# Kernel tuning notes

Measured on AMD Instinct MI355X. Metric: run time of the kernel, lower is better.

## Reference

```python
import jax, jax.numpy as jnp
import numpy as np

B, S, ENC_D, DEC_D, ATTN_D, OUT_D = 32, 2048, 1024, 1024, 1024, 1024
SCALING = 1.0


def setup_inputs() -> dict:
    key = jax.random.key(0)
    ks = jax.random.split(key, 10)
    enc_states = jax.random.normal(ks[0], (B, S, ENC_D), dtype=jnp.float32)
    # lengths in [S//2, S] so every row has at least one valid position
    enc_len = jax.random.randint(ks[1], (B,), S // 2, S + 1, dtype=jnp.int32)
    dec_states = jax.random.normal(ks[2], (B, DEC_D), dtype=jnp.float32)
    s = 0.02
    W_enc = jax.random.normal(ks[3], (ENC_D, ATTN_D), dtype=jnp.float32) * s
    b_enc = jnp.zeros((ATTN_D,), dtype=jnp.float32)
    W_dec = jax.random.normal(ks[4], (DEC_D, ATTN_D), dtype=jnp.float32) * s
    b_dec = jnp.zeros((ATTN_D,), dtype=jnp.float32)
    w_attn = jax.random.normal(ks[5], (ATTN_D,), dtype=jnp.float32) * s
    W_out = jax.random.normal(ks[6], (ENC_D, OUT_D), dtype=jnp.float32) * s
    b_out = jnp.zeros((OUT_D,), dtype=jnp.float32)
    return {
        "enc_states": enc_states,
        "dec_states": dec_states,
        "W_enc": W_enc, "b_enc": b_enc,
        "W_dec": W_dec, "b_dec": b_dec,
        "w_attn": w_attn,
        "W_out": W_out, "b_out": b_out,
        "enc_len": enc_len,
    }


def reference(enc_states, dec_states, W_enc, b_enc, W_dec, b_dec, w_attn, W_out, b_out, enc_len):
    # precomputed_enc_h = mlp_enc(enc_states): [B, S, ATTN_D]
    enc_h = jnp.einsum("bse,ea->bsa", enc_states, W_enc) + b_enc
    # dec_h = mlp_dec(dec_states): [B, ATTN_D]
    dec_h = dec_states @ W_dec + b_dec
    # additive (Bahdanau) score: tanh(enc_h + dec_h) . w_attn -> [B, S]
    attn = jnp.einsum("bsa,a->bs", jnp.tanh(enc_h + dec_h[:, None, :]), w_attn)
    # length mask
    mask = jnp.arange(enc_states.shape[1])[None, :] < enc_len[:, None]  # [B, S]
    attn = jnp.where(mask, attn, -jnp.inf)
    attn = jax.nn.softmax(attn * SCALING, axis=-1)
    # context = attn @ enc_states -> [B, ENC_D]
    context = jnp.einsum("bs,bse->be", attn, enc_states)
    context = context @ W_out + b_out
    return (context, attn)
```

## Files before the change

kernel.cpp:

```cpp
#include <hip/hip_runtime.h>
#include <cstdint>
#include <cstddef>

#define BATCH 32
#define SEQ   2048
#define DIM   1024
#define MROWS (BATCH*SEQ)

typedef __attribute__((ext_vector_type(4))) float  floatx4;
typedef __attribute__((ext_vector_type(8))) short  short8;

__device__ __forceinline__ unsigned short f2bf(float f) {
  unsigned int u = __float_as_uint(f);
  u += 0x7fffu + ((u >> 16) & 1u);
  return (unsigned short)(u >> 16);
}

__device__ __forceinline__ void async16(const void* g, void* l) {
  __builtin_amdgcn_global_load_lds(
      (const __attribute__((address_space(1))) unsigned int*)g,
      (__attribute__((address_space(3))) unsigned int*)l, 16, 0, 0);
}

__device__ __forceinline__ float fast_tanh(float x) {
  float e = __expf(2.0f * x);
  return 1.0f - 2.0f * __builtin_amdgcn_rcpf(1.0f + e);
}

__global__ void k_convert(const float* __restrict__ enc, const int* __restrict__ enc_len,
                          unsigned short* __restrict__ Abf) {
  int b = blockIdx.y;
  int r0 = blockIdx.x * 8;
  if (r0 >= enc_len[b]) return;
  size_t base = ((size_t)b * SEQ + r0) * DIM;
  const float4* src = (const float4*)(enc + base);
  ushort4* dst = (ushort4*)(Abf + base);
  int tid = threadIdx.x;
#pragma unroll
  for (int i = 0; i < 8; ++i) {
    float4 v = src[tid + i * 256];
    ushort4 h;
    h.x = f2bf(v.x); h.y = f2bf(v.y); h.z = f2bf(v.z); h.w = f2bf(v.w);
    dst[tid + i * 256] = h;
  }
}

__global__ void k_transpose(const float* __restrict__ W, unsigned short* __restrict__ Wt) {
  __shared__ float tile[32][33];
  int n0 = blockIdx.x * 32, k0 = blockIdx.y * 32;
  int tx = threadIdx.x, ty = threadIdx.y;
#pragma unroll
  for (int i = 0; i < 4; ++i) {
    int y = ty + i * 8;
    tile[y][tx] = W[(size_t)(k0 + y) * DIM + n0 + tx];
  }
  __syncthreads();
#pragma unroll
  for (int i = 0; i < 4; ++i) {
    int y = ty + i * 8;
    Wt[(size_t)(n0 + y) * DIM + k0 + tx] = f2bf(tile[tx][y]);
  }
}

__global__ void k_dech(const float* __restrict__ dec, const float* __restrict__ W_dec,
                       const float* __restrict__ b_dec, const float* __restrict__ b_enc,
                       float* __restrict__ dech) {
  int a  = blockIdx.x * 256 + threadIdx.x;
  int bg = blockIdx.y * 8;
  int z  = blockIdx.z;
  float bias = (z == 0) ? (b_dec[a] + b_enc[a]) : 0.0f;
  float acc[8];
#pragma unroll
  for (int j = 0; j < 8; ++j) acc[j] = bias;
  const float* wc = W_dec + (size_t)z * 128 * DIM + a;
#pragma unroll 4
  for (int e = 0; e < 128; ++e) {
    float w = wc[(size_t)e * DIM];
#pragma unroll
    for (int j = 0; j < 8; ++j)
      acc[j] = fmaf(dec[(size_t)(bg + j) * DIM + z * 128 + e], w, acc[j]);
  }
#pragma unroll
  for (int j = 0; j < 8; ++j)
    atomicAdd(&dech[(size_t)(bg + j) * DIM + a], acc[j]);
}

#define PH_BAR do { asm volatile("" ::: "memory"); __builtin_amdgcn_s_barrier(); asm volatile("" ::: "memory"); } while(0)
#define SCHED0 __builtin_amdgcn_sched_barrier(0)
#define SP1 __builtin_amdgcn_s_setprio(1)
#define SP0 __builtin_amdgcn_s_setprio(0)
#define VMCNT(n) asm volatile("s_waitcnt vmcnt(" #n ")" ::: "memory")

__global__ void __launch_bounds__(512, 2) k_gemm256(
    const unsigned short* __restrict__ Abf,
    const unsigned short* __restrict__ Wt,
    const float* __restrict__ dech,
    const float* __restrict__ w_attn,
    const int* __restrict__ enc_len,
    float* __restrict__ score)
{
  int bid = blockIdx.x;
  int t  = (bid & 7) * 128 + (bid >> 3);
  int nb = t & 3;
  int rt = t >> 2;
  int bb = rt >> 3;
  int len = enc_len[bb];
  if (((rt & 7) * 256) >= len) return;

  __shared__ __align__(16) char lds[131072];

  int tid = threadIdx.x;
  int w = tid >> 6, lane = tid & 63;
  int wr = w >> 2;
  int wc = w & 3;
  int li = lane & 15, g = lane >> 4;
  int xl = (li & 7) << 4;

  const char* Ag = (const char*)(Abf + (size_t)rt * 256 * DIM);
  const char* Bg = (const char*)(Wt  + (size_t)nb * 256 * DIM);

  size_t sbase = (size_t)((lane >> 3) * 2048 +
                 (((lane & 7) << 4) ^ (((lane >> 3) & 7) << 4)));
  size_t swoff = (size_t)(w * 2) * 16384;
  int    ldbase = w * 2048;

#define STAGE_A(buf, h, kt) do { \
  async16(Ag + sbase + swoff + (size_t)(h) * 262144 + (size_t)(kt) * 128, \
          lds + (buf) * 32768 + ldbase + (h) * 16384); \
  async16(Ag + sbase + swoff + 16384 + (size_t)(h) * 262144 + (size_t)(kt) * 128, \
          lds + (buf) * 32768 + ldbase + 1024 + (h) * 16384); \
} while (0)
#define STAGE_B(buf, h, kt) do { \
  async16(Bg + sbase + swoff + (size_t)(h) * 262144 + (size_t)(kt) * 128, \
          lds + 65536 + (buf) * 32768 + ldbase + (h) * 16384); \
  async16(Bg + sbase + swoff + 16384 + (size_t)(h) * 262144 + (size_t)(kt) * 128, \
          lds + 65536 + (buf) * 32768 + ldbase + 1024 + (h) * 16384); \
} while (0)

  short8 sA0[2][2], sA1[2][2];
  short8 aX[2][2];
  short8 bX[2][2];
  floatx4 acc[8][4] = {};

#define RD_A2(buf, f0, DST) do { \
  const char* base_ = lds + (buf) * 32768 + (wr * 128 + (f0) * 16 + li) * 128; \
  int c0_ = (g * 16) ^ xl; \
  _Pragma("unroll") for (int j = 0; j < 2; ++j) { \
    DST[j][0] = *(const short8*)(base_ + j * 2048 + c0_); \
    DST[j][1] = *(const short8*)(base_ + j * 2048 + (c0_ ^ 64)); \
  } \
} while (0)
#define RD_B(buf, nh, DST) do { \
  const char* base_ = lds + 65536 + (buf) * 32768 + (wc * 64 + (nh) * 32 + li) * 128; \
  int c0_ = (g * 16) ^ xl; \
  _Pragma("unroll") for (int tnq = 0; tnq < 2; ++tnq) { \
    DST[tnq][0] = *(const short8*)(base_ + tnq * 2048 + c0_); \
    DST[tnq][1] = *(const short8*)(base_ + tnq * 2048 + (c0_ ^ 64)); \
  } \
} while (0)
#define MFMA_Q(mh, nh, ALO, AHI, BB) do { \
  _Pragma("unroll") for (int ks = 0; ks < 2; ++ks) \
  _Pragma("unroll") for (int tnq = 0; tnq < 2; ++tnq) { \
    acc[(mh)*4+0][(nh)*2+tnq] = __builtin_amdgcn_mfma_f32_16x16x32_bf16(ALO[0][ks], BB[tnq][ks], acc[(mh)*4+0][(nh)*2+tnq], 0, 0, 0); \
    acc[(mh)*4+1][(nh)*2+tnq] = __builtin_amdgcn_mfma_f32_16x16x32_bf16(ALO[1][ks], BB[tnq][ks], acc[(mh)*4+1][(nh)*2+tnq], 0, 0, 0); \
    acc[(mh)*4+2][(nh)*2+tnq] = __builtin_amdgcn_mfma_f32_16x16x32_bf16(AHI[0][ks], BB[tnq][ks], acc[(mh)*4+2][(nh)*2+tnq], 0, 0, 0); \
    acc[(mh)*4+3][(nh)*2+tnq] = __builtin_amdgcn_mfma_f32_16x16x32_bf16(AHI[1][ks], BB[tnq][ks], acc[(mh)*4+3][(nh)*2+tnq], 0, 0, 0); \
  } \
} while (0)

#define TILE_STEP(CUR, KT2, MODE, SP_, SQ_) do { \
   \
  RD_A2(CUR, 2, aX); \
  RD_B(CUR, 0, bX); \
  PH_BAR; SCHED0; SP1; MFMA_Q(0, 0, SP_, aX, bX); SP0; SCHED0; \
  PH_BAR; \
   \
  RD_B(CUR, 1, SQ_); \
  PH_BAR; SCHED0; SP1; MFMA_Q(0, 1, SP_, aX, SQ_); SP0; SCHED0; \
  PH_BAR; \
   \
  if ((MODE) == 0) { STAGE_B(CUR, 0, KT2); STAGE_B(CUR, 1, KT2); } \
  RD_A2(CUR, 4, SP_); \
  RD_A2(CUR, 6, aX); \
  PH_BAR; SCHED0; SP1; MFMA_Q(1, 1, SP_, aX, SQ_); SP0; SCHED0; \
  PH_BAR; \
   \
  if ((MODE) == 0) { STAGE_A(CUR, 0, KT2); STAGE_A(CUR, 1, KT2); } \
  if ((MODE) == 0) { VMCNT(8); } else if ((MODE) == 1) { VMCNT(0); } \
  if ((MODE) < 2) RD_A2((CUR) ^ 1, 0, SQ_); \
  PH_BAR; SCHED0; SP1; MFMA_Q(1, 0, SP_, aX, bX); SP0; SCHED0; \
  PH_BAR; \
} while (0)

  STAGE_B(0, 0, 0); STAGE_B(0, 1, 0); STAGE_A(0, 0, 0); STAGE_A(0, 1, 0);
  STAGE_B(1, 0, 1); STAGE_B(1, 1, 1); STAGE_A(1, 0, 1); STAGE_A(1, 1, 1);
  VMCNT(8);
  PH_BAR;
  RD_A2(0, 0, sA0);

#pragma unroll 1
  for (int u = 0; u < 14; u += 2) {
    TILE_STEP(0, u + 2, 0, sA0, sA1);
    TILE_STEP(1, u + 3, 0, sA1, sA0);
  }
  TILE_STEP(0, 0, 1, sA0, sA1);
  TILE_STEP(1, 0, 2, sA1, sA0);

  float dh[4], wa[4];
#pragma unroll
  for (int tn = 0; tn < 4; ++tn) {
    int n = nb * 256 + wc * 64 + tn * 16 + li;
    dh[tn] = dech[(size_t)bb * DIM + n];
    wa[tn] = w_attn[n];
  }
#pragma unroll
  for (int tm = 0; tm < 8; ++tm) {
    int mrow = rt * 256 + wr * 128 + tm * 16 + g * 4;
#pragma unroll
    for (int r = 0; r < 4; ++r) {
      float v = 0.0f;
#pragma unroll
      for (int tn = 0; tn < 4; ++tn)
        v = fmaf(wa[tn], fast_tanh(acc[tm][tn][r] + dh[tn]), v);
      v += __shfl_xor(v, 1);
      v += __shfl_xor(v, 2);
      v += __shfl_xor(v, 4);
      v += __shfl_xor(v, 8);
      if (li == 0) atomicAdd(&score[mrow + r], v);
    }
  }
#undef TILE_STEP
#undef MFMA_Q
#undef RD_B
#undef RD_A2
#undef STAGE_B
#undef STAGE_A
}

__global__ void __launch_bounds__(256, 2) k_gemm_f32(
    const float* __restrict__ A, const unsigned short* __restrict__ Wt,
    const float* __restrict__ dech, const float* __restrict__ w_attn,
    const int* __restrict__ enc_len, float* __restrict__ score)
{
  int linear = blockIdx.x;
  int xcd = linear & 7;
  int j   = linear >> 3;
  int rb  = xcd * 64 + (j >> 3);
  int nb  = j & 7;
  int bb  = rb >> 4;
  int len = enc_len[bb];
  if (((rb & 15) * 128) >= len) return;

  __shared__ __align__(16) unsigned short sA[128 * 40];
  __shared__ __align__(16) unsigned short sB[128 * 32];

  int tid  = threadIdx.x;
  int w    = tid >> 6, lane = tid & 63;
  int wm   = (w >> 1) * 64, wn = (w & 1) * 64;
  int li   = lane & 15, g = lane >> 4;

  const float*          Abase = A  + (size_t)rb * 128 * DIM;
  const unsigned short* Bbase = Wt + (size_t)nb * 128 * DIM;

  floatx4 acc[4][4] = {};

  for (int kb = 0; kb < 32; ++kb) {
    __syncthreads();
#pragma unroll
    for (int i = 0; i < 2; ++i) {
      int c  = (w * 2 + i) * 64 + lane;
      int n  = c >> 2;
      int kh = (c & 3) ^ ((n >> 1) & 3);
      async16(Bbase + (size_t)n * DIM + kb * 32 + kh * 8, (char*)sB + (w * 2 + i) * 1024);
    }
#pragma unroll
    for (int i = 0; i < 4; ++i) {
      int f4  = tid + i * 256;
      int row = f4 >> 3, kq = f4 & 7;
      float4 v = *(const float4*)(Abase + (size_t)row * DIM + kb * 32 + kq * 4);
      ushort4 h;
      h.x = f2bf(v.x); h.y = f2bf(v.y); h.z = f2bf(v.z); h.w = f2bf(v.w);
      *(ushort4*)&sA[row * 40 + kq * 4] = h;
    }
    __syncthreads();

    short8 af[4], bfr[4];
#pragma unroll
    for (int t = 0; t < 4; ++t) {
      int row = wm + t * 16 + li;
      af[t] = *(const short8*)&sA[row * 40 + g * 8];
      int nl = wn + t * 16 + li;
      int phys = (nl << 2) | (g ^ ((nl >> 1) & 3));
      bfr[t] = *(const short8*)((const char*)sB + phys * 16);
    }
#pragma unroll
    for (int tm = 0; tm < 4; ++tm)
#pragma unroll
      for (int tn = 0; tn < 4; ++tn)
        acc[tm][tn] = __builtin_amdgcn_mfma_f32_16x16x32_bf16(af[tm], bfr[tn], acc[tm][tn], 0, 0, 0);
  }

  float dh[4], wa[4];
#pragma unroll
  for (int tn = 0; tn < 4; ++tn) {
    int n = nb * 128 + wn + tn * 16 + li;
    dh[tn] = dech[(size_t)bb * DIM + n];
    wa[tn] = w_attn[n];
  }
#pragma unroll
  for (int tm = 0; tm < 4; ++tm) {
    int mrow = rb * 128 + wm + tm * 16 + g * 4;
#pragma unroll
    for (int r = 0; r < 4; ++r) {
      float v = 0.0f;
#pragma unroll
      for (int tn = 0; tn < 4; ++tn)
        v = fmaf(wa[tn], fast_tanh(acc[tm][tn][r] + dh[tn]), v);
      v += __shfl_xor(v, 1);
      v += __shfl_xor(v, 2);
      v += __shfl_xor(v, 4);
      v += __shfl_xor(v, 8);
      if (li == 0) atomicAdd(&score[mrow + r], v);
    }
  }
}

__global__ void k_softmax(const float* __restrict__ score, const int* __restrict__ enc_len,
                          float* __restrict__ attn) {
  int b = blockIdx.x, tid = threadIdx.x;
  int len = enc_len[b];
  __shared__ float red[256];
  float v[8];
  float m = -1e30f;
#pragma unroll
  for (int i = 0; i < 8; ++i) {
    int s = tid + i * 256;
    v[i] = score[(size_t)b * SEQ + s];
    if (s < len) m = fmaxf(m, v[i]);
  }
  red[tid] = m; __syncthreads();
  for (int st = 128; st > 0; st >>= 1) {
    if (tid < st) red[tid] = fmaxf(red[tid], red[tid + st]);
    __syncthreads();
  }
  float mx = red[0]; __syncthreads();
  float sum = 0.0f;
#pragma unroll
  for (int i = 0; i < 8; ++i) {
    int s = tid + i * 256;
    float e = (s < len) ? __expf(v[i] - mx) : 0.0f;
    v[i] = e; sum += e;
  }
  red[tid] = sum; __syncthreads();
  for (int st = 128; st > 0; st >>= 1) {
    if (tid < st) red[tid] += red[tid + st];
    __syncthreads();
  }
  float inv = 1.0f / red[0];
#pragma unroll
  for (int i = 0; i < 8; ++i)
    attn[(size_t)b * SEQ + tid + i * 256] = v[i] * inv;
}

__global__ void k_context(const float* __restrict__ enc, const float* __restrict__ attn,
                          const int* __restrict__ enc_len, float* __restrict__ ctx) {
  int b = blockIdx.y, sc = blockIdx.x;
  int len = enc_len[b];
  int s0 = sc * 32;
  if (s0 >= len) return;
  int cnt = min(32, len - s0);
  int tid = threadIdx.x;
  const float* base = enc + ((size_t)b * SEQ + s0) * DIM + tid * 4;
  const float* ap   = attn + (size_t)b * SEQ + s0;
  float a0 = 0.f, a1 = 0.f, a2 = 0.f, a3 = 0.f;
  int i = 0;
  for (; i + 8 <= cnt; i += 8) {
    float4 x[8];
    float  w[8];
#pragma unroll
    for (int u = 0; u < 8; ++u)
      x[u] = *(const float4*)(base + (size_t)(i + u) * DIM);
#pragma unroll
    for (int u = 0; u < 8; ++u)
      w[u] = ap[i + u];
#pragma unroll
    for (int u = 0; u < 8; ++u) {
      a0 = fmaf(w[u], x[u].x, a0); a1 = fmaf(w[u], x[u].y, a1);
      a2 = fmaf(w[u], x[u].z, a2); a3 = fmaf(w[u], x[u].w, a3);
    }
  }
  for (; i < cnt; ++i) {
    float w = ap[i];
    float4 x = *(const float4*)(base + (size_t)i * DIM);
    a0 = fmaf(w, x.x, a0); a1 = fmaf(w, x.y, a1);
    a2 = fmaf(w, x.z, a2); a3 = fmaf(w, x.w, a3);
  }
  float* c = ctx + (size_t)b * DIM + tid * 4;
  atomicAdd(c + 0, a0); atomicAdd(c + 1, a1);
  atomicAdd(c + 2, a2); atomicAdd(c + 3, a3);
}

__global__ void k_out(const float* __restrict__ ctx, const float* __restrict__ W_out,
                      const float* __restrict__ b_out, float* __restrict__ out) {
  int o  = blockIdx.x * 256 + threadIdx.x;
  int bg = blockIdx.y * 8;
  int z  = blockIdx.z;
  float bias = (z == 0) ? b_out[o] : 0.0f;
  float acc[8];
#pragma unroll
  for (int j = 0; j < 8; ++j) acc[j] = bias;
  const float* wc = W_out + (size_t)z * 128 * DIM + o;
#pragma unroll 4
  for (int e = 0; e < 128; ++e) {
    float w = wc[(size_t)e * DIM];
#pragma unroll
    for (int j = 0; j < 8; ++j)
      acc[j] = fmaf(ctx[(size_t)(bg + j) * DIM + z * 128 + e], w, acc[j]);
  }
#pragma unroll
  for (int j = 0; j < 8; ++j)
    atomicAdd(&out[(size_t)(bg + j) * DIM + o], acc[j]);
}

extern "C" void kernel_launch(void* const* d_in, const int* in_sizes, int n_in,
                              void* d_out, int out_size, void* d_ws, size_t ws_size,
                              hipStream_t stream) {
  (void)in_sizes; (void)n_in; (void)out_size;
  const float* enc_states = (const float*)d_in[0];
  const float* dec_states = (const float*)d_in[1];
  const float* W_enc      = (const float*)d_in[2];
  const float* b_enc      = (const float*)d_in[3];
  const float* W_dec      = (const float*)d_in[4];
  const float* b_dec      = (const float*)d_in[5];
  const float* w_attn     = (const float*)d_in[6];
  const float* W_out      = (const float*)d_in[7];
  const float* b_out      = (const float*)d_in[8];
  const int*   enc_len    = (const int*)  d_in[9];

  float* out_ctx  = (float*)d_out;
  float* out_attn = (float*)d_out + BATCH * DIM;

  char* ws = (char*)d_ws;
  unsigned short* Wt  = (unsigned short*)ws;
  float* score = (float*)(ws + (2u << 20));
  float* ctx   = (float*)(ws + (2u << 20) + 262144);
  float* dech  = (float*)(ws + (2u << 20) + 262144 + 131072);
  unsigned short* Abf = (unsigned short*)(ws + (3u << 20));
  const bool fast = ws_size >= ((size_t)(3u << 20) + ((size_t)MROWS * DIM * 2));

  hipMemsetAsync(ws + (2u << 20), 0, 262144 + 131072 + 131072, stream);
  hipMemsetAsync(d_out, 0, (size_t)BATCH * DIM * sizeof(float), stream);

  k_transpose<<<dim3(32, 32), dim3(32, 8), 0, stream>>>(W_enc, Wt);
  k_dech<<<dim3(4, 4, 8), 256, 0, stream>>>(dec_states, W_dec, b_dec, b_enc, dech);
  if (fast) {
    k_convert<<<dim3(SEQ / 8, BATCH), 256, 0, stream>>>(enc_states, enc_len, Abf);
    k_gemm256<<<1024, 512, 0, stream>>>(Abf, Wt, dech, w_attn, enc_len, score);
  } else {
    k_gemm_f32<<<4096, 256, 0, stream>>>(enc_states, Wt, dech, w_attn, enc_len, score);
  }
  k_softmax<<<BATCH, 256, 0, stream>>>(score, enc_len, out_attn);
  k_context<<<dim3(64, BATCH), 256, 0, stream>>>(enc_states, out_attn, enc_len, ctx);
  k_out<<<dim3(4, 4, 8), 256, 0, stream>>>(ctx, W_out, b_out, out_ctx);
}
```

Before: 611.8 us.

## Fuse prep kernels into one launch and split GEMM into two column-half launches

Merges the weight transpose, decoder projection and bf16 conversion of encoder states into a single k_prep launch that dispatches on block index, removing two kernel launches and their serialization gaps. The main GEMM is split into two launches of 512 blocks, each covering half of the N column tiles, with block-to-tile remapping adjusted. Splitting the GEMM may improve L2 reuse of the weight half per launch but adds a launch and re-reads the A rows twice.

```diff
diff --git a/kernel.cpp b/kernel.cpp
--- a/kernel.cpp
+++ b/kernel.cpp
@@ -27,21 +27,64 @@
   return 1.0f - 2.0f * __builtin_amdgcn_rcpf(1.0f + e);
 }
 
-__global__ void k_convert(const float* __restrict__ enc, const int* __restrict__ enc_len,
-                          unsigned short* __restrict__ Abf) {
-  int b = blockIdx.y;
-  int r0 = blockIdx.x * 8;
-  if (r0 >= enc_len[b]) return;
-  size_t base = ((size_t)b * SEQ + r0) * DIM;
-  const float4* src = (const float4*)(enc + base);
-  ushort4* dst = (ushort4*)(Abf + base);
+__global__ void k_prep(const float* __restrict__ enc, const int* __restrict__ enc_len,
+                       unsigned short* __restrict__ Abf,
+                       const float* __restrict__ W_enc, unsigned short* __restrict__ Wt,
+                       const float* __restrict__ dec, const float* __restrict__ W_dec,
+                       const float* __restrict__ b_dec, const float* __restrict__ b_enc,
+                       float* __restrict__ dech) {
+  __shared__ float tile[32][33];
+  int blk = blockIdx.x;
   int tid = threadIdx.x;
-#pragma unroll
-  for (int i = 0; i < 8; ++i) {
-    float4 v = src[tid + i * 256];
-    ushort4 h;
-    h.x = f2bf(v.x); h.y = f2bf(v.y); h.z = f2bf(v.z); h.w = f2bf(v.w);
-    dst[tid + i * 256] = h;
+  if (blk < 1024) {
+    int n0 = (blk & 31) * 32, k0 = (blk >> 5) * 32;
+    int tx = tid & 31, ty = tid >> 5;
+#pragma unroll
+    for (int i = 0; i < 4; ++i) {
+      int y = ty + i * 8;
+      tile[y][tx] = W_enc[(size_t)(k0 + y) * DIM + n0 + tx];
+    }
+    __syncthreads();
+#pragma unroll
+    for (int i = 0; i < 4; ++i) {
+      int y = ty + i * 8;
+      Wt[(size_t)(n0 + y) * DIM + k0 + tx] = f2bf(tile[tx][y]);
+    }
+  } else if (blk < 1152) {
+    int db = blk - 1024;
+    int ax = db & 3, bgi = (db >> 2) & 3, z = db >> 4;
+    int a  = ax * 256 + tid;
+    int bg = bgi * 8;
+    float bias = (z == 0) ? (b_dec[a] + b_enc[a]) : 0.0f;
+    float acc[8];
+#pragma unroll
+    for (int j = 0; j < 8; ++j) acc[j] = bias;
+    const float* wcp = W_dec + (size_t)z * 128 * DIM + a;
+#pragma unroll 4
+    for (int e = 0; e < 128; ++e) {
+      float w = wcp[(size_t)e * DIM];
+#pragma unroll
+      for (int j = 0; j < 8; ++j)
+        acc[j] = fmaf(dec[(size_t)(bg + j) * DIM + z * 128 + e], w, acc[j]);
+    }
+#pragma unroll
+    for (int j = 0; j < 8; ++j)
+      atomicAdd(&dech[(size_t)(bg + j) * DIM + a], acc[j]);
+  } else {
+    int cv = blk - 1152;
+    int b = cv >> 8, rc = cv & 255;
+    int r0 = rc * 8;
+    if (r0 >= enc_len[b]) return;
+    size_t base = ((size_t)b * SEQ + r0) * DIM;
+    const float4* src = (const float4*)(enc + base);
+    ushort4* dst = (ushort4*)(Abf + base);
+#pragma unroll
+    for (int i = 0; i < 8; ++i) {
+      float4 v = src[tid + i * 256];
+      ushort4 h;
+      h.x = f2bf(v.x); h.y = f2bf(v.y); h.z = f2bf(v.z); h.w = f2bf(v.w);
+      dst[tid + i * 256] = h;
+    }
   }
 }
 
@@ -97,12 +140,13 @@
     const float* __restrict__ dech,
     const float* __restrict__ w_attn,
     const int* __restrict__ enc_len,
-    float* __restrict__ score)
+    float* __restrict__ score,
+    int nbase)
 {
   int bid = blockIdx.x;
-  int t  = (bid & 7) * 128 + (bid >> 3);
-  int nb = t & 3;
-  int rt = t >> 2;
+  int t  = (bid & 7) * 64 + (bid >> 3);
+  int nb = nbase + (t & 1);
+  int rt = t >> 1;
   int bb = rt >> 3;
   int len = enc_len[bb];
   if (((rt & 7) * 256) >= len) return;
@@ -169,22 +213,18 @@
 } while (0)
 
 #define TILE_STEP(CUR, KT2, MODE, SP_, SQ_) do { \
-   \
   RD_A2(CUR, 2, aX); \
   RD_B(CUR, 0, bX); \
   PH_BAR; SCHED0; SP1; MFMA_Q(0, 0, SP_, aX, bX); SP0; SCHED0; \
   PH_BAR; \
-   \
   RD_B(CUR, 1, SQ_); \
   PH_BAR; SCHED0; SP1; MFMA_Q(0, 1, SP_, aX, SQ_); SP0; SCHED0; \
   PH_BAR; \
-   \
   if ((MODE) == 0) { STAGE_B(CUR, 0, KT2); STAGE_B(CUR, 1, KT2); } \
   RD_A2(CUR, 4, SP_); \
   RD_A2(CUR, 6, aX); \
   PH_BAR; SCHED0; SP1; MFMA_Q(1, 1, SP_, aX, SQ_); SP0; SCHED0; \
   PH_BAR; \
-   \
   if ((MODE) == 0) { STAGE_A(CUR, 0, KT2); STAGE_A(CUR, 1, KT2); } \
   if ((MODE) == 0) { VMCNT(8); } else if ((MODE) == 1) { VMCNT(0); } \
   if ((MODE) < 2) RD_A2((CUR) ^ 1, 0, SQ_); \
@@ -451,12 +491,14 @@
   hipMemsetAsync(ws + (2u << 20), 0, 262144 + 131072 + 131072, stream);
   hipMemsetAsync(d_out, 0, (size_t)BATCH * DIM * sizeof(float), stream);
 
-  k_transpose<<<dim3(32, 32), dim3(32, 8), 0, stream>>>(W_enc, Wt);
-  k_dech<<<dim3(4, 4, 8), 256, 0, stream>>>(dec_states, W_dec, b_dec, b_enc, dech);
   if (fast) {
-    k_convert<<<dim3(SEQ / 8, BATCH), 256, 0, stream>>>(enc_states, enc_len, Abf);
-    k_gemm256<<<1024, 512, 0, stream>>>(Abf, Wt, dech, w_attn, enc_len, score);
+    k_prep<<<9344, 256, 0, stream>>>(enc_states, enc_len, Abf,
+                                     W_enc, Wt, dec_states, W_dec, b_dec, b_enc, dech);
+    k_gemm256<<<512, 512, 0, stream>>>(Abf, Wt, dech, w_attn, enc_len, score, 0);
+    k_gemm256<<<512, 512, 0, stream>>>(Abf, Wt, dech, w_attn, enc_len, score, 2);
   } else {
+    k_transpose<<<dim3(32, 32), dim3(32, 8), 0, stream>>>(W_enc, Wt);
+    k_dech<<<dim3(4, 4, 8), 256, 0, stream>>>(dec_states, W_dec, b_dec, b_enc, dech);
     k_gemm_f32<<<4096, 256, 0, stream>>>(enc_states, Wt, dech, w_attn, enc_len, score);
   }
   k_softmax<<<BATCH, 256, 0, stream>>>(score, enc_len, out_attn);
```

Result: faster. 583.6 us (-4.6%).

## Fuse fp32-to-bf16 conversion of encoder states into GEMM A-tile loading

Applied to the files above, without the earlier changes.

Drops the separate conversion pass that wrote a bf16 copy of enc_states. The GEMM now loads fp32 A tiles into registers, converts them to bf16 and writes them into LDS inside the software pipeline. The weight transpose and decoder projection are merged into one prep launch, and the fp32 fallback GEMM is removed. This removes a full read and write of the large activation tensor plus a launch. In exchange the GEMM reads twice the bytes for A, uses more registers, and converts in the main loop where async global-to-LDS copies were used before.

```diff
diff --git a/kernel.cpp b/kernel.cpp
--- a/kernel.cpp
+++ b/kernel.cpp
@@ -27,62 +27,48 @@
   return 1.0f - 2.0f * __builtin_amdgcn_rcpf(1.0f + e);
 }
 
-__global__ void k_convert(const float* __restrict__ enc, const int* __restrict__ enc_len,
-                          unsigned short* __restrict__ Abf) {
-  int b = blockIdx.y;
-  int r0 = blockIdx.x * 8;
-  if (r0 >= enc_len[b]) return;
-  size_t base = ((size_t)b * SEQ + r0) * DIM;
-  const float4* src = (const float4*)(enc + base);
-  ushort4* dst = (ushort4*)(Abf + base);
-  int tid = threadIdx.x;
-#pragma unroll
-  for (int i = 0; i < 8; ++i) {
-    float4 v = src[tid + i * 256];
-    ushort4 h;
-    h.x = f2bf(v.x); h.y = f2bf(v.y); h.z = f2bf(v.z); h.w = f2bf(v.w);
-    dst[tid + i * 256] = h;
-  }
-}
-
-__global__ void k_transpose(const float* __restrict__ W, unsigned short* __restrict__ Wt) {
-  __shared__ float tile[32][33];
-  int n0 = blockIdx.x * 32, k0 = blockIdx.y * 32;
-  int tx = threadIdx.x, ty = threadIdx.y;
-#pragma unroll
-  for (int i = 0; i < 4; ++i) {
-    int y = ty + i * 8;
-    tile[y][tx] = W[(size_t)(k0 + y) * DIM + n0 + tx];
-  }
-  __syncthreads();
-#pragma unroll
-  for (int i = 0; i < 4; ++i) {
-    int y = ty + i * 8;
-    Wt[(size_t)(n0 + y) * DIM + k0 + tx] = f2bf(tile[tx][y]);
-  }
-}
-
-__global__ void k_dech(const float* __restrict__ dec, const float* __restrict__ W_dec,
+__global__ void k_prep(const float* __restrict__ W_enc, unsigned short* __restrict__ Wt,
+                       const float* __restrict__ dec, const float* __restrict__ W_dec,
                        const float* __restrict__ b_dec, const float* __restrict__ b_enc,
                        float* __restrict__ dech) {
-  int a  = blockIdx.x * 256 + threadIdx.x;
-  int bg = blockIdx.y * 8;
-  int z  = blockIdx.z;
-  float bias = (z == 0) ? (b_dec[a] + b_enc[a]) : 0.0f;
-  float acc[8];
-#pragma unroll
-  for (int j = 0; j < 8; ++j) acc[j] = bias;
-  const float* wc = W_dec + (size_t)z * 128 * DIM + a;
+  __shared__ float tile[32][33];
+  int blk = blockIdx.x;
+  int tid = threadIdx.x;
+  if (blk < 1024) {
+    int n0 = (blk & 31) * 32, k0 = (blk >> 5) * 32;
+    int tx = tid & 31, ty = tid >> 5;
+#pragma unroll
+    for (int i = 0; i < 4; ++i) {
+      int y = ty + i * 8;
+      tile[y][tx] = W_enc[(size_t)(k0 + y) * DIM + n0 + tx];
+    }
+    __syncthreads();
+#pragma unroll
+    for (int i = 0; i < 4; ++i) {
+      int y = ty + i * 8;
+      Wt[(size_t)(n0 + y) * DIM + k0 + tx] = f2bf(tile[tx][y]);
+    }
+  } else {
+    int db = blk - 1024;
+    int ax = db & 3, bgi = (db >> 2) & 3, z = db >> 4;
+    int a  = ax * 256 + tid;
+    int bg = bgi * 8;
+    float bias = (z == 0) ? (b_dec[a] + b_enc[a]) : 0.0f;
+    float acc[8];
+#pragma unroll
+    for (int j = 0; j < 8; ++j) acc[j] = bias;
+    const float* wcp = W_dec + (size_t)z * 128 * DIM + a;
 #pragma unroll 4
-  for (int e = 0; e < 128; ++e) {
-    float w = wc[(size_t)e * DIM];
+    for (int e = 0; e < 128; ++e) {
+      float w = wcp[(size_t)e * DIM];
+#pragma unroll
+      for (int j = 0; j < 8; ++j)
+        acc[j] = fmaf(dec[(size_t)(bg + j) * DIM + z * 128 + e], w, acc[j]);
+    }
 #pragma unroll
     for (int j = 0; j < 8; ++j)
-      acc[j] = fmaf(dec[(size_t)(bg + j) * DIM + z * 128 + e], w, acc[j]);
-  }
-#pragma unroll
-  for (int j = 0; j < 8; ++j)
-    atomicAdd(&dech[(size_t)(bg + j) * DIM + a], acc[j]);
+      atomicAdd(&dech[(size_t)(bg + j) * DIM + a], acc[j]);
+  }
 }
 
 #define PH_BAR do { asm volatile("" ::: "memory"); __builtin_amdgcn_s_barrier(); asm volatile("" ::: "memory"); } while(0)
@@ -90,9 +76,10 @@
 #define SP1 __builtin_amdgcn_s_setprio(1)
 #define SP0 __builtin_amdgcn_s_setprio(0)
 #define VMCNT(n) asm volatile("s_waitcnt vmcnt(" #n ")" ::: "memory")
+#define LGKM0 asm volatile("s_waitcnt lgkmcnt(0)" ::: "memory")
 
 __global__ void __launch_bounds__(512, 2) k_gemm256(
-    const unsigned short* __restrict__ Abf,
+    const float* __restrict__ enc,
     const unsigned short* __restrict__ Wt,
     const float* __restrict__ dech,
     const float* __restrict__ w_attn,
@@ -116,25 +103,50 @@
   int li = lane & 15, g = lane >> 4;
   int xl = (li & 7) << 4;
 
-  const char* Ag = (const char*)(Abf + (size_t)rt * 256 * DIM);
-  const char* Bg = (const char*)(Wt  + (size_t)nb * 256 * DIM);
+  const char* Agc = (const char*)enc + (size_t)rt * 256 * 4096;
+  const char* Bg  = (const char*)(Wt + (size_t)nb * 256 * DIM);
 
   size_t sbase = (size_t)((lane >> 3) * 2048 +
                  (((lane & 7) << 4) ^ (((lane >> 3) & 7) << 4)));
   size_t swoff = (size_t)(w * 2) * 16384;
   int    ldbase = w * 2048;
 
-#define STAGE_A(buf, h, kt) do { \
-  async16(Ag + sbase + swoff + (size_t)(h) * 262144 + (size_t)(kt) * 128, \
-          lds + (buf) * 32768 + ldbase + (h) * 16384); \
-  async16(Ag + sbase + swoff + 16384 + (size_t)(h) * 262144 + (size_t)(kt) * 128, \
-          lds + (buf) * 32768 + ldbase + 1024 + (h) * 16384); \
-} while (0)
 #define STAGE_B(buf, h, kt) do { \
   async16(Bg + sbase + swoff + (size_t)(h) * 262144 + (size_t)(kt) * 128, \
           lds + 65536 + (buf) * 32768 + ldbase + (h) * 16384); \
   async16(Bg + sbase + swoff + 16384 + (size_t)(h) * 262144 + (size_t)(kt) * 128, \
           lds + 65536 + (buf) * 32768 + ldbase + 1024 + (h) * 16384); \
+} while (0)
+
+  size_t aoff = (size_t)(w * 16 + (lane >> 3)) * 4096 +
+                (size_t)(((lane & 7) ^ (lane >> 3)) * 32);
+  float4 aR[2][2][2];
+
+#define LOAD_A(kt) do { \
+  _Pragma("unroll") for (int c = 0; c < 2; ++c) { \
+    const char* g0_ = Agc + aoff + (size_t)(c * 8) * 4096 + (size_t)(kt) * 256; \
+    aR[0][c][0] = *(const float4*)(g0_); \
+    aR[0][c][1] = *(const float4*)(g0_ + 16); \
+  } \
+} while (0)
+#define LOAD_A1(kt) do { \
+  _Pragma("unroll") for (int c = 0; c < 2; ++c) { \
+    const char* g1_ = Agc + aoff + (size_t)(128 + c * 8) * 4096 + (size_t)(kt) * 256; \
+    aR[1][c][0] = *(const float4*)(g1_); \
+    aR[1][c][1] = *(const float4*)(g1_ + 16); \
+  } \
+} while (0)
+#define WRITE_A(buf) do { \
+  _Pragma("unroll") for (int h_ = 0; h_ < 2; ++h_) \
+  _Pragma("unroll") for (int c_ = 0; c_ < 2; ++c_) { \
+    float4 u0_ = aR[h_][c_][0], u1_ = aR[h_][c_][1]; \
+    short8 pk_; \
+    pk_[0] = (short)f2bf(u0_.x); pk_[1] = (short)f2bf(u0_.y); \
+    pk_[2] = (short)f2bf(u0_.z); pk_[3] = (short)f2bf(u0_.w); \
+    pk_[4] = (short)f2bf(u1_.x); pk_[5] = (short)f2bf(u1_.y); \
+    pk_[6] = (short)f2bf(u1_.z); pk_[7] = (short)f2bf(u1_.w); \
+    *(short8*)(lds + (buf) * 32768 + h_ * 16384 + w * 2048 + c_ * 1024 + lane * 16) = pk_; \
+  } \
 } while (0)
 
   short8 sA0[2][2], sA1[2][2];
@@ -172,10 +184,12 @@
    \
   RD_A2(CUR, 2, aX); \
   RD_B(CUR, 0, bX); \
+  if ((MODE) == 0) { LOAD_A(KT2); } \
   PH_BAR; SCHED0; SP1; MFMA_Q(0, 0, SP_, aX, bX); SP0; SCHED0; \
   PH_BAR; \
    \
   RD_B(CUR, 1, SQ_); \
+  if ((MODE) == 0) { LOAD_A1(KT2); } \
   PH_BAR; SCHED0; SP1; MFMA_Q(0, 1, SP_, aX, SQ_); SP0; SCHED0; \
   PH_BAR; \
    \
@@ -185,16 +199,22 @@
   PH_BAR; SCHED0; SP1; MFMA_Q(1, 1, SP_, aX, SQ_); SP0; SCHED0; \
   PH_BAR; \
    \
-  if ((MODE) == 0) { STAGE_A(CUR, 0, KT2); STAGE_A(CUR, 1, KT2); } \
-  if ((MODE) == 0) { VMCNT(8); } else if ((MODE) == 1) { VMCNT(0); } \
+  if ((MODE) == 0) { VMCNT(4); WRITE_A(CUR); } \
+  else if ((MODE) == 1) { VMCNT(0); } \
   if ((MODE) < 2) RD_A2((CUR) ^ 1, 0, SQ_); \
   PH_BAR; SCHED0; SP1; MFMA_Q(1, 0, SP_, aX, bX); SP0; SCHED0; \
   PH_BAR; \
 } while (0)
 
-  STAGE_B(0, 0, 0); STAGE_B(0, 1, 0); STAGE_A(0, 0, 0); STAGE_A(0, 1, 0);
-  STAGE_B(1, 0, 1); STAGE_B(1, 1, 1); STAGE_A(1, 0, 1); STAGE_A(1, 1, 1);
-  VMCNT(8);
+  LOAD_A(0); LOAD_A1(0);
+  VMCNT(0);
+  WRITE_A(0);
+  LOAD_A(1); LOAD_A1(1);
+  STAGE_B(0, 0, 0); STAGE_B(0, 1, 0);
+  STAGE_B(1, 0, 1); STAGE_B(1, 1, 1);
+  VMCNT(4);
+  WRITE_A(1);
+  LGKM0;
   PH_BAR;
   RD_A2(0, 0, sA0);
 
@@ -233,96 +253,10 @@
 #undef MFMA_Q
 #undef RD_B
 #undef RD_A2
+#undef WRITE_A
+#undef LOAD_A1
+#undef LOAD_A
 #undef STAGE_B
-#undef STAGE_A
-}
-
-__global__ void __launch_bounds__(256, 2) k_gemm_f32(
-    const float* __restrict__ A, const unsigned short* __restrict__ Wt,
-    const float* __restrict__ dech, const float* __restrict__ w_attn,
-    const int* __restrict__ enc_len, float* __restrict__ score)
-{
-  int linear = blockIdx.x;
-  int xcd = linear & 7;
-  int j   = linear >> 3;
-  int rb  = xcd * 64 + (j >> 3);
-  int nb  = j & 7;
-  int bb  = rb >> 4;
-  int len = enc_len[bb];
-  if (((rb & 15) * 128) >= len) return;
-
-  __shared__ __align__(16) unsigned short sA[128 * 40];
-  __shared__ __align__(16) unsigned short sB[128 * 32];
-
-  int tid  = threadIdx.x;
-  int w    = tid >> 6, lane = tid & 63;
-  int wm   = (w >> 1) * 64, wn = (w & 1) * 64;
-  int li   = lane & 15, g = lane >> 4;
-
-  const float*          Abase = A  + (size_t)rb * 128 * DIM;
-  const unsigned short* Bbase = Wt + (size_t)nb * 128 * DIM;
-
-  floatx4 acc[4][4] = {};
-
-  for (int kb = 0; kb < 32; ++kb) {
-    __syncthreads();
-#pragma unroll
-    for (int i = 0; i < 2; ++i) {
-      int c  = (w * 2 + i) * 64 + lane;
-      int n  = c >> 2;
-      int kh = (c & 3) ^ ((n >> 1) & 3);
-      async16(Bbase + (size_t)n * DIM + kb * 32 + kh * 8, (char*)sB + (w * 2 + i) * 1024);
-    }
-#pragma unroll
-    for (int i = 0; i < 4; ++i) {
-      int f4  = tid + i * 256;
-      int row = f4 >> 3, kq = f4 & 7;
-      float4 v = *(const float4*)(Abase + (size_t)row * DIM + kb * 32 + kq * 4);
-      ushort4 h;
-      h.x = f2bf(v.x); h.y = f2bf(v.y); h.z = f2bf(v.z); h.w = f2bf(v.w);
-      *(ushort4*)&sA[row * 40 + kq * 4] = h;
-    }
-    __syncthreads();
-
-    short8 af[4], bfr[4];
-#pragma unroll
-    for (int t = 0; t < 4; ++t) {
-      int row = wm + t * 16 + li;
-      af[t] = *(const short8*)&sA[row * 40 + g * 8];
-      int nl = wn + t * 16 + li;
-      int phys = (nl << 2) | (g ^ ((nl >> 1) & 3));
-      bfr[t] = *(const short8*)((const char*)sB + phys * 16);
-    }
-#pragma unroll
-    for (int tm = 0; tm < 4; ++tm)
-#pragma unroll
-      for (int tn = 0; tn < 4; ++tn)
-        acc[tm][tn] = __builtin_amdgcn_mfma_f32_16x16x32_bf16(af[tm], bfr[tn], acc[tm][tn], 0, 0, 0);
-  }
-
-  float dh[4], wa[4];
-#pragma unroll
-  for (int tn = 0; tn < 4; ++tn) {
-    int n = nb * 128 + wn + tn * 16 + li;
-    dh[tn] = dech[(size_t)bb * DIM + n];
-    wa[tn] = w_attn[n];
-  }
-#pragma unroll
-  for (int tm = 0; tm < 4; ++tm) {
-    int mrow = rb * 128 + wm + tm * 16 + g * 4;
-#pragma unroll
-    for (int r = 0; r < 4; ++r) {
-      float v = 0.0f;
-#pragma unroll
-      for (int tn = 0; tn < 4; ++tn)
-        v = fmaf(wa[tn], fast_tanh(acc[tm][tn][r] + dh[tn]), v);
-      v += __shfl_xor(v, 1);
-      v += __shfl_xor(v, 2);
-      v += __shfl_xor(v, 4);
-      v += __shfl_xor(v, 8);
-      if (li == 0) atomicAdd(&score[mrow + r], v);
-    }
-  }
 }
 
 __global__ void k_softmax(const float* __restrict__ score, const int* __restrict__ enc_len,
@@ -425,7 +359,7 @@
 extern "C" void kernel_launch(void* const* d_in, const int* in_sizes, int n_in,
                               void* d_out, int out_size, void* d_ws, size_t ws_size,
                               hipStream_t stream) {
-  (void)in_sizes; (void)n_in; (void)out_size;
+  (void)in_sizes; (void)n_in; (void)out_size; (void)ws_size;
   const float* enc_states = (const float*)d_in[0];
   const float* dec_states = (const float*)d_in[1];
   const float* W_enc      = (const float*)d_in[2];
@@ -445,20 +379,12 @@
   float* score = (float*)(ws + (2u << 20));
   float* ctx   = (float*)(ws + (2u << 20) + 262144);
   float* dech  = (float*)(ws + (2u << 20) + 262144 + 131072);
-  unsigned short* Abf = (unsigned short*)(ws + (3u << 20));
-  const bool fast = ws_size >= ((size_t)(3u << 20) + ((size_t)MROWS * DIM * 2));
 
   hipMemsetAsync(ws + (2u << 20), 0, 262144 + 131072 + 131072, stream);
   hipMemsetAsync(d_out, 0, (size_t)BATCH * DIM * sizeof(float), stream);
 
-  k_transpose<<<dim3(32, 32), dim3(32, 8), 0, stream>>>(W_enc, Wt);
-  k_dech<<<dim3(4, 4, 8), 256, 0, stream>>>(dec_states, W_dec, b_dec, b_enc, dech);
-  if (fast) {
-    k_convert<<<dim3(SEQ / 8, BATCH), 256, 0, stream>>>(enc_states, enc_len, Abf);
-    k_gemm256<<<1024, 512, 0, stream>>>(Abf, Wt, dech, w_attn, enc_len, score);
-  } else {
-    k_gemm_f32<<<4096, 256, 0, stream>>>(enc_states, Wt, dech, w_attn, enc_len, score);
-  }
+  k_prep<<<1152, 256, 0, stream>>>(W_enc, Wt, dec_states, W_dec, b_dec, b_enc, dech);
+  k_gemm256<<<1024, 512, 0, stream>>>(enc_states, Wt, dech, w_attn, enc_len, score);
   k_softmax<<<BATCH, 256, 0, stream>>>(score, enc_len, out_attn);
   k_context<<<dim3(64, BATCH), 256, 0, stream>>>(enc_states, out_attn, enc_len, ctx);
   k_out<<<dim3(4, 4, 8), 256, 0, stream>>>(ctx, W_out, b_out, out_ctx);
```

Result: slower. 671.8 us (+9.8%).
